# Kernel optimization log

Hardware: AMD Instinct MI355X
Metric: run time of the kernel (lower is better)

The kernel has to match this reference:

```python
import jax, jax.numpy as jnp
import numpy as np

N, P, C = 8, 256, 128


def setup_inputs() -> dict:
    key = jax.random.key(0)
    ks = jax.random.split(key, 16)
    s = lambda k, shape, fan_in: jax.random.normal(k, shape, jnp.float32) / np.sqrt(fan_in)
    return {
        "x": jax.random.normal(ks[0], (N, P, C), jnp.float32),
        "pos": jax.random.normal(ks[1], (N, P, P, 2), jnp.float32),
        # projections (no bias), stored (in, out)
        "Wq": s(ks[2], (C, C), C),
        "Wk": s(ks[3], (C, C), C),
        "Wv": s(ks[4], (C, C), C),
        # qk_mlp: Linear(C,C) -> ReLU -> Linear(C,1)
        "W1": s(ks[5], (C, C), C),
        "b1": jnp.zeros((C,), jnp.float32),
        "W2": s(ks[6], (C, 1), C),
        "b2": jnp.zeros((1,), jnp.float32),
        # pos_mlp: Linear(2,C) -> ReLU -> Linear(C,C)
        "Wp1": s(ks[7], (2, C), 2),
        "bp1": jnp.zeros((C,), jnp.float32),
        "Wp2": s(ks[8], (C, C), C),
        "bp2": jnp.zeros((C,), jnp.float32),
    }


def reference(x, pos, Wq, Wk, Wv, W1, b1, W2, b2, Wp1, bp1, Wp2, bp2):
    # x: [N,P,C], pos: [N,P,P,2]
    q = x @ Wq  # [N,P,C]
    k = x @ Wk
    v = x @ Wv
    pos_emb = jax.nn.relu(pos @ Wp1 + bp1) @ Wp2 + bp2  # [N,P,P,C]
    # diff[n,a,b,:] = q[n,b] - k[n,a] + pos_emb[n,a,b]
    diff = q[:, None, :, :] - k[:, :, None, :] + pos_emb  # [N,P,P,C]
    att = (jax.nn.relu(diff @ W1 + b1) @ W2 + b2)[..., 0]  # [N,P,P]
    att = jax.nn.softmax(att, axis=-1)
    # out[n,a] = sum_b att[n,a,b] * v[n,b]
    fuse = jnp.einsum("nab,nbc->nac", att, v)
    return x + fuse
```

## Files before the change

### kernel.cpp

```cpp
#include <hip/hip_runtime.h>
#include <hip/hip_bf16.h>

#define NB 8
#define PP 256
#define CC 128
#define APAD 136
#define XS 132

typedef __attribute__((ext_vector_type(8))) unsigned short ushort8;
typedef __bf16 bf16x8 __attribute__((ext_vector_type(8)));
typedef float float4v __attribute__((ext_vector_type(4)));

__device__ __forceinline__ float bf2f(unsigned short u) {
    union { unsigned int i; float f; } x; x.i = ((unsigned int)u) << 16; return x.f;
}
__device__ __forceinline__ unsigned short f2bf(float f) {
    union { float f; unsigned int i; } x; x.f = f;
    unsigned int r = x.i + 0x7fffu + ((x.i >> 16) & 1u);
    return (unsigned short)(r >> 16);
}
__device__ __forceinline__ unsigned int pk2(float a, float b) {
    return (unsigned int)f2bf(a) | ((unsigned int)f2bf(b) << 16);
}

__global__ void prep_kernel(const float* __restrict__ Wq, const float* __restrict__ Wk,
                            const float* __restrict__ Wp2, const float* __restrict__ W1,
                            const float* __restrict__ b1, const float* __restrict__ bp2,
                            float* __restrict__ Wq1, float* __restrict__ Wk1,
                            unsigned short* __restrict__ W21t, float* __restrict__ bvec) {
    int bx = blockIdx.x, j = threadIdx.x;
    __shared__ float xr[CC];
    if (bx < 384) {
        int r = bx & 127;
        const float* X = (bx < 128) ? Wq : (bx < 256) ? Wk : Wp2;
        xr[j] = X[r * CC + j];
        __syncthreads();
        float s = 0.f;
#pragma unroll 4
        for (int t = 0; t < CC; ++t) s = fmaf(xr[t], W1[t * CC + j], s);
        if (bx < 128)      Wq1[r * CC + j] = s;
        else if (bx < 256) Wk1[r * CC + j] = s;
        else               W21t[j * CC + r] = f2bf(s);
    } else {
        float s = b1[j];
        for (int c = 0; c < CC; ++c) s = fmaf(bp2[c], W1[c * CC + j], s);
        bvec[j] = s;
    }
}

__global__ __launch_bounds__(256) void qkv_kernel(
    const float* __restrict__ x, const float* __restrict__ Wq1,
    const float* __restrict__ Wk1, const float* __restrict__ Wv,
    unsigned short* __restrict__ qwtb, float* __restrict__ kw,
    float* __restrict__ v) {
    __shared__ float Ws[CC * CC];
    __shared__ float xs[32 * XS];
    int t = threadIdx.x, which = blockIdx.y;
    const float* W = (which == 0) ? Wq1 : (which == 1) ? Wk1 : Wv;
    int row0 = blockIdx.x * 32;
#pragma unroll 8
    for (int i = 0; i < 64; ++i) Ws[i * 256 + t] = W[i * 256 + t];
#pragma unroll 4
    for (int i = 0; i < 16; ++i) {
        int idx = i * 256 + t;
        int r = idx >> 7, c = idx & 127;
        xs[r * XS + c] = x[(size_t)(row0 + r) * CC + c];
    }
    __syncthreads();
    int tc = t & 31, tr = t >> 5;
    int j0 = tc * 4, r0 = tr * 4;
    float acc[4][4];
#pragma unroll
    for (int i = 0; i < 4; ++i)
#pragma unroll
        for (int jj = 0; jj < 4; ++jj) acc[i][jj] = 0.f;
#pragma unroll 2
    for (int c = 0; c < CC; ++c) {
        float4 w4 = *(const float4*)&Ws[c * CC + j0];
        float x0 = xs[(r0 + 0) * XS + c], x1 = xs[(r0 + 1) * XS + c];
        float x2 = xs[(r0 + 2) * XS + c], x3 = xs[(r0 + 3) * XS + c];
        acc[0][0] = fmaf(x0, w4.x, acc[0][0]); acc[0][1] = fmaf(x0, w4.y, acc[0][1]);
        acc[0][2] = fmaf(x0, w4.z, acc[0][2]); acc[0][3] = fmaf(x0, w4.w, acc[0][3]);
        acc[1][0] = fmaf(x1, w4.x, acc[1][0]); acc[1][1] = fmaf(x1, w4.y, acc[1][1]);
        acc[1][2] = fmaf(x1, w4.z, acc[1][2]); acc[1][3] = fmaf(x1, w4.w, acc[1][3]);
        acc[2][0] = fmaf(x2, w4.x, acc[2][0]); acc[2][1] = fmaf(x2, w4.y, acc[2][1]);
        acc[2][2] = fmaf(x2, w4.z, acc[2][2]); acc[2][3] = fmaf(x2, w4.w, acc[2][3]);
        acc[3][0] = fmaf(x3, w4.x, acc[3][0]); acc[3][1] = fmaf(x3, w4.y, acc[3][1]);
        acc[3][2] = fmaf(x3, w4.z, acc[3][2]); acc[3][3] = fmaf(x3, w4.w, acc[3][3]);
    }
    if (which == 0) {
        int n = row0 >> 8, b0 = row0 & 255;
#pragma unroll
        for (int jj = 0; jj < 4; ++jj) {
            ushort4 pk;
            pk.x = f2bf(acc[0][jj]); pk.y = f2bf(acc[1][jj]);
            pk.z = f2bf(acc[2][jj]); pk.w = f2bf(acc[3][jj]);
            *(ushort4*)(qwtb + (size_t)(n * CC + j0 + jj) * PP + b0 + r0) = pk;
        }
    } else {
        float* o = (which == 1) ? kw : v;
#pragma unroll
        for (int i = 0; i < 4; ++i)
            *(float4*)&o[(size_t)(row0 + r0 + i) * CC + j0] =
                make_float4(acc[i][0], acc[i][1], acc[i][2], acc[i][3]);
    }
}

__global__ __launch_bounds__(256, 3) void attn_kernel(
    const float* __restrict__ x, const float* __restrict__ pos,
    const float* __restrict__ Wp1, const float* __restrict__ bp1,
    const float* __restrict__ W2, const float* __restrict__ b2,
    const unsigned short* __restrict__ W21t, const float* __restrict__ bvec,
    const unsigned short* __restrict__ qwtb, const float* __restrict__ kw,
    const float* __restrict__ v, float* __restrict__ out)
{
    __shared__ __attribute__((aligned(16))) unsigned short Bs[128 * APAD];
    __shared__ float p0s[PP], p1s[PP];
    __shared__ float wa[CC], wb[CC], bpv[CC];
    __shared__ float logits[PP];
    __shared__ float red[8];
    __shared__ float avred[CC];

    const int t = threadIdx.x;
    const int n = blockIdx.x >> 8, a = blockIdx.x & 255;
    const int lane = t & 63, wv = t >> 6;
    const int ln = lane & 15, quad = lane >> 4;

    if (t < CC) {
        wa[t]  = Wp1[t];
        wb[t]  = Wp1[CC + t];
        bpv[t] = bp1[t];
    }
    {
        const float2* pr = (const float2*)(pos + (size_t)(n * PP + a) * PP * 2);
        float2 pp = pr[t];
        p0s[t] = pp.x;
        p1s[t] = pp.y;
    }
    {
        int j = t >> 1, p = t & 1;
        const ushort8* src = (const ushort8*)(W21t + j * CC + p * 64);
        ushort8* dst = (ushort8*)(Bs + j * APAD + p * 64);
#pragma unroll
        for (int i = 0; i < 8; ++i) dst[i] = src[i];
    }
    const float b2f = b2[0];

    float w2v[8], kbv[8];
    {
        const float* kwrow = kw + (size_t)(n * PP + a) * CC;
#pragma unroll
        for (int nt = 0; nt < 8; ++nt) {
            int j = nt * 16 + ln;
            w2v[nt] = W2[j];
            kbv[nt] = bvec[j] - kwrow[j];
        }
    }
    __syncthreads();

#pragma unroll 1
    for (int chunk = 0; chunk < 4; ++chunk) {
        const int rbase = chunk * 64 + wv * 16;
        const float P0 = p0s[rbase + ln];
        const float P1 = p1s[rbase + ln];

        ushort4 qv4[8];
#pragma unroll
        for (int nt = 0; nt < 8; ++nt)
            qv4[nt] = *(const ushort4*)(qwtb + (size_t)(n * CC + nt * 16 + ln) * PP
                                        + rbase + quad * 4);

        float4v acc[8];
#pragma unroll
        for (int j = 0; j < 8; ++j) acc[j] = (float4v)0.f;

#pragma unroll 1
        for (int kk = 0; kk < 128; kk += 32) {
            const int ko = kk + quad * 8;
            float4 a0 = *(const float4*)&wa[ko],  a1 = *(const float4*)&wa[ko + 4];
            float4 c0 = *(const float4*)&wb[ko],  c1 = *(const float4*)&wb[ko + 4];
            float4 d0 = *(const float4*)&bpv[ko], d1 = *(const float4*)&bpv[ko + 4];
            float h0 = fmaxf(fmaf(P0, a0.x, fmaf(P1, c0.x, d0.x)), 0.f);
            float h1 = fmaxf(fmaf(P0, a0.y, fmaf(P1, c0.y, d0.y)), 0.f);
            float h2 = fmaxf(fmaf(P0, a0.z, fmaf(P1, c0.z, d0.z)), 0.f);
            float h3 = fmaxf(fmaf(P0, a0.w, fmaf(P1, c0.w, d0.w)), 0.f);
            float h4 = fmaxf(fmaf(P0, a1.x, fmaf(P1, c1.x, d1.x)), 0.f);
            float h5 = fmaxf(fmaf(P0, a1.y, fmaf(P1, c1.y, d1.y)), 0.f);
            float h6 = fmaxf(fmaf(P0, a1.z, fmaf(P1, c1.z, d1.z)), 0.f);
            float h7 = fmaxf(fmaf(P0, a1.w, fmaf(P1, c1.w, d1.w)), 0.f);
            union { bf16x8 v8; unsigned int u[4]; } cv;
            cv.u[0] = pk2(h0, h1); cv.u[1] = pk2(h2, h3);
            cv.u[2] = pk2(h4, h5); cv.u[3] = pk2(h6, h7);
            bf16x8 af = cv.v8;
#pragma unroll
            for (int j = 0; j < 8; ++j) {
                bf16x8 bfr = *(const bf16x8*)(Bs + (j * 16 + ln) * APAD + ko);
                acc[j] = __builtin_amdgcn_mfma_f32_16x16x32_bf16(af, bfr, acc[j], 0, 0, 0);
            }
        }

        float s0 = 0.f, s1 = 0.f, s2 = 0.f, s3 = 0.f;
#pragma unroll
        for (int nt = 0; nt < 8; ++nt) {
            float kb = kbv[nt], w2 = w2v[nt];
            s0 = fmaf(fmaxf(acc[nt][0] + bf2f(qv4[nt].x) + kb, 0.f), w2, s0);
            s1 = fmaf(fmaxf(acc[nt][1] + bf2f(qv4[nt].y) + kb, 0.f), w2, s1);
            s2 = fmaf(fmaxf(acc[nt][2] + bf2f(qv4[nt].z) + kb, 0.f), w2, s2);
            s3 = fmaf(fmaxf(acc[nt][3] + bf2f(qv4[nt].w) + kb, 0.f), w2, s3);
        }
        float sr[4] = {s0, s1, s2, s3};
#pragma unroll
        for (int r = 0; r < 4; ++r) {
            float s = sr[r];
            s += __shfl_xor(s, 1);
            s += __shfl_xor(s, 2);
            s += __shfl_xor(s, 4);
            s += __shfl_xor(s, 8);
            if (ln == 0) logits[rbase + quad * 4 + r] = s + b2f;
        }
    }
    __syncthreads();

    float lv = logits[t];
    float wm = lv;
#pragma unroll
    for (int d = 1; d < 64; d <<= 1) wm = fmaxf(wm, __shfl_xor(wm, d));
    if (lane == 0) red[wv] = wm;
    __syncthreads();
    float m = fmaxf(fmaxf(red[0], red[1]), fmaxf(red[2], red[3]));
    float e = __expf(lv - m);
    float es = e;
#pragma unroll
    for (int d = 1; d < 64; d <<= 1) es += __shfl_xor(es, d);
    if (lane == 0) red[4 + wv] = es;
    __syncthreads();
    float denom = red[4] + red[5] + red[6] + red[7];
    logits[t] = e / denom;
    __syncthreads();

    int c = t & 127, h2 = t >> 7;
    const float* vp = v + (size_t)(n * PP + h2 * 128) * CC + c;
    float acc0 = 0.f;
#pragma unroll 8
    for (int b = 0; b < 128; ++b)
        acc0 = fmaf(logits[h2 * 128 + b], vp[(size_t)b * CC], acc0);
    if (h2 == 1) avred[c] = acc0;
    __syncthreads();
    if (h2 == 0) {
        int oidx = (n * PP + a) * CC + c;
        out[oidx] = x[oidx] + acc0 + avred[c];
    }
}

extern "C" void kernel_launch(void* const* d_in, const int* in_sizes, int n_in,
                              void* d_out, int out_size, void* d_ws, size_t ws_size,
                              hipStream_t stream) {
    const float* x   = (const float*)d_in[0];
    const float* pos = (const float*)d_in[1];
    const float* Wq  = (const float*)d_in[2];
    const float* Wk  = (const float*)d_in[3];
    const float* Wv  = (const float*)d_in[4];
    const float* W1  = (const float*)d_in[5];
    const float* b1  = (const float*)d_in[6];
    const float* W2  = (const float*)d_in[7];
    const float* b2  = (const float*)d_in[8];
    const float* Wp1 = (const float*)d_in[9];
    const float* bp1 = (const float*)d_in[10];
    const float* Wp2 = (const float*)d_in[11];
    const float* bp2 = (const float*)d_in[12];
    float* out = (float*)d_out;

    float* ws   = (float*)d_ws;
    float* Wq1  = ws;
    float* Wk1  = Wq1 + 16384;
    float* bvec = Wk1 + 16384;
    float* kw   = bvec + 128;
    float* v    = kw + 262144;
    unsigned short* qwtb = (unsigned short*)(v + 262144);
    unsigned short* W21t = qwtb + 262144;

    prep_kernel<<<385, 128, 0, stream>>>(Wq, Wk, Wp2, W1, b1, bp2, Wq1, Wk1, W21t, bvec);
    qkv_kernel<<<dim3(64, 3), 256, 0, stream>>>(x, Wq1, Wk1, Wv, qwtb, kw, v);
    attn_kernel<<<NB * PP, 256, 0, stream>>>(x, pos, Wp1, bp1, W2, b2,
                                             W21t, bvec, qwtb, kw, v, out);
}
```

Before: 158.7 us.

## Switch pos-MLP hidden to packed fp16 with pre-swizzled f16 MFMA weights

The pos-MLP first layer is now computed with packed half2 math, with weights held in registers. The combined W2·W1 matrix is stored in fp16, pre-swizzled by the prep kernel into MFMA fragment order, so the attention kernel can copy it linearly into LDS and read conflict-free without padding. This drops the fp32 FMA and bf16 rounding work and the strided LDS loads. The final attention-times-V step now splits the b dimension over 8 groups with float4 loads and reduces them through shared memory. The main risk is lower precision for pos and hidden values in fp16, plus higher register pressure from the per-thread weight arrays.

```diff
diff --git a/kernel.cpp b/kernel.cpp
--- a/kernel.cpp
+++ b/kernel.cpp
@@ -4,11 +4,11 @@
 #define NB 8
 #define PP 256
 #define CC 128
-#define APAD 136
 #define XS 132
 
 typedef __attribute__((ext_vector_type(8))) unsigned short ushort8;
-typedef __bf16 bf16x8 __attribute__((ext_vector_type(8)));
+typedef _Float16 f16x8 __attribute__((ext_vector_type(8)));
+typedef _Float16 h2v __attribute__((ext_vector_type(2)));
 typedef float float4v __attribute__((ext_vector_type(4)));
 
 __device__ __forceinline__ float bf2f(unsigned short u) {
@@ -19,15 +19,12 @@
     unsigned int r = x.i + 0x7fffu + ((x.i >> 16) & 1u);
     return (unsigned short)(r >> 16);
 }
-__device__ __forceinline__ unsigned int pk2(float a, float b) {
-    return (unsigned int)f2bf(a) | ((unsigned int)f2bf(b) << 16);
-}
 
 __global__ void prep_kernel(const float* __restrict__ Wq, const float* __restrict__ Wk,
                             const float* __restrict__ Wp2, const float* __restrict__ W1,
                             const float* __restrict__ b1, const float* __restrict__ bp2,
                             float* __restrict__ Wq1, float* __restrict__ Wk1,
-                            unsigned short* __restrict__ W21t, float* __restrict__ bvec) {
+                            unsigned short* __restrict__ W21f, float* __restrict__ bvec) {
     int bx = blockIdx.x, j = threadIdx.x;
     __shared__ float xr[CC];
     if (bx < 384) {
@@ -40,7 +37,15 @@
         for (int t = 0; t < CC; ++t) s = fmaf(xr[t], W1[t * CC + j], s);
         if (bx < 128)      Wq1[r * CC + j] = s;
         else if (bx < 256) Wk1[r * CC + j] = s;
-        else               W21t[j * CC + r] = f2bf(s);
+        else {
+            int k = r;
+            int kk = k >> 5, quad = (k >> 3) & 3, e = k & 7;
+            int jt = j >> 4, ln = j & 15;
+            int lane = quad * 16 + ln;
+            union { _Float16 h; unsigned short u; } cv;
+            cv.h = (_Float16)s;
+            W21f[(((kk * 8 + jt) * 64) + lane) * 8 + e] = cv.u;
+        }
     } else {
         float s = b1[j];
         for (int c = 0; c < CC; ++c) s = fmaf(bp2[c], W1[c * CC + j], s);
@@ -110,27 +115,21 @@
     const float* __restrict__ x, const float* __restrict__ pos,
     const float* __restrict__ Wp1, const float* __restrict__ bp1,
     const float* __restrict__ W2, const float* __restrict__ b2,
-    const unsigned short* __restrict__ W21t, const float* __restrict__ bvec,
+    const unsigned short* __restrict__ W21f, const float* __restrict__ bvec,
     const unsigned short* __restrict__ qwtb, const float* __restrict__ kw,
     const float* __restrict__ v, float* __restrict__ out)
 {
-    __shared__ __attribute__((aligned(16))) unsigned short Bs[128 * APAD];
+    __shared__ __attribute__((aligned(16))) unsigned short Bs[128 * 128];
     __shared__ float p0s[PP], p1s[PP];
-    __shared__ float wa[CC], wb[CC], bpv[CC];
     __shared__ float logits[PP];
     __shared__ float red[8];
-    __shared__ float avred[CC];
+    __shared__ float avp[8 * 128];
 
     const int t = threadIdx.x;
     const int n = blockIdx.x >> 8, a = blockIdx.x & 255;
     const int lane = t & 63, wv = t >> 6;
     const int ln = lane & 15, quad = lane >> 4;
 
-    if (t < CC) {
-        wa[t]  = Wp1[t];
-        wb[t]  = Wp1[CC + t];
-        bpv[t] = bp1[t];
-    }
     {
         const float2* pr = (const float2*)(pos + (size_t)(n * PP + a) * PP * 2);
         float2 pp = pr[t];
@@ -138,13 +137,23 @@
         p1s[t] = pp.y;
     }
     {
-        int j = t >> 1, p = t & 1;
-        const ushort8* src = (const ushort8*)(W21t + j * CC + p * 64);
-        ushort8* dst = (ushort8*)(Bs + j * APAD + p * 64);
-#pragma unroll
-        for (int i = 0; i < 8; ++i) dst[i] = src[i];
+        const uint4* src = (const uint4*)W21f;
+        uint4* dst = (uint4*)Bs;
+#pragma unroll
+        for (int i = 0; i < 8; ++i) dst[i * 256 + t] = src[i * 256 + t];
     }
     const float b2f = b2[0];
+
+    h2v wa2[16], wb2[16], bp2h[16];
+#pragma unroll
+    for (int kk = 0; kk < 4; ++kk)
+#pragma unroll
+        for (int p = 0; p < 4; ++p) {
+            int k = kk * 32 + quad * 8 + p * 2;
+            wa2[kk * 4 + p]  = (h2v){(_Float16)Wp1[k],      (_Float16)Wp1[k + 1]};
+            wb2[kk * 4 + p]  = (h2v){(_Float16)Wp1[CC + k], (_Float16)Wp1[CC + k + 1]};
+            bp2h[kk * 4 + p] = (h2v){(_Float16)bp1[k],      (_Float16)bp1[k + 1]};
+        }
 
     float w2v[8], kbv[8];
     {
@@ -156,13 +165,16 @@
             kbv[nt] = bvec[j] - kwrow[j];
         }
     }
+    const h2v z2 = (h2v){(_Float16)0.f, (_Float16)0.f};
     __syncthreads();
 
 #pragma unroll 1
     for (int chunk = 0; chunk < 4; ++chunk) {
         const int rbase = chunk * 64 + wv * 16;
-        const float P0 = p0s[rbase + ln];
-        const float P1 = p1s[rbase + ln];
+        const _Float16 p0h = (_Float16)p0s[rbase + ln];
+        const _Float16 p1h = (_Float16)p1s[rbase + ln];
+        const h2v P0h = (h2v){p0h, p0h};
+        const h2v P1h = (h2v){p1h, p1h};
 
         ushort4 qv4[8];
 #pragma unroll
@@ -175,27 +187,16 @@
         for (int j = 0; j < 8; ++j) acc[j] = (float4v)0.f;
 
 #pragma unroll 1
-        for (int kk = 0; kk < 128; kk += 32) {
-            const int ko = kk + quad * 8;
-            float4 a0 = *(const float4*)&wa[ko],  a1 = *(const float4*)&wa[ko + 4];
-            float4 c0 = *(const float4*)&wb[ko],  c1 = *(const float4*)&wb[ko + 4];
-            float4 d0 = *(const float4*)&bpv[ko], d1 = *(const float4*)&bpv[ko + 4];
-            float h0 = fmaxf(fmaf(P0, a0.x, fmaf(P1, c0.x, d0.x)), 0.f);
-            float h1 = fmaxf(fmaf(P0, a0.y, fmaf(P1, c0.y, d0.y)), 0.f);
-            float h2 = fmaxf(fmaf(P0, a0.z, fmaf(P1, c0.z, d0.z)), 0.f);
-            float h3 = fmaxf(fmaf(P0, a0.w, fmaf(P1, c0.w, d0.w)), 0.f);
-            float h4 = fmaxf(fmaf(P0, a1.x, fmaf(P1, c1.x, d1.x)), 0.f);
-            float h5 = fmaxf(fmaf(P0, a1.y, fmaf(P1, c1.y, d1.y)), 0.f);
-            float h6 = fmaxf(fmaf(P0, a1.z, fmaf(P1, c1.z, d1.z)), 0.f);
-            float h7 = fmaxf(fmaf(P0, a1.w, fmaf(P1, c1.w, d1.w)), 0.f);
-            union { bf16x8 v8; unsigned int u[4]; } cv;
-            cv.u[0] = pk2(h0, h1); cv.u[1] = pk2(h2, h3);
-            cv.u[2] = pk2(h4, h5); cv.u[3] = pk2(h6, h7);
-            bf16x8 af = cv.v8;
+        for (int kk = 0; kk < 4; ++kk) {
+            union { f16x8 v8; h2v h2[4]; } A;
+#pragma unroll
+            for (int p = 0; p < 4; ++p)
+                A.h2[p] = __builtin_elementwise_max(
+                    P0h * wa2[kk * 4 + p] + P1h * wb2[kk * 4 + p] + bp2h[kk * 4 + p], z2);
 #pragma unroll
             for (int j = 0; j < 8; ++j) {
-                bf16x8 bfr = *(const bf16x8*)(Bs + (j * 16 + ln) * APAD + ko);
-                acc[j] = __builtin_amdgcn_mfma_f32_16x16x32_bf16(af, bfr, acc[j], 0, 0, 0);
+                f16x8 bfr = *(const f16x8*)(Bs + (((kk * 8 + j) * 64) + lane) * 8);
+                acc[j] = __builtin_amdgcn_mfma_f32_16x16x32_f16(A.v8, bfr, acc[j], 0, 0, 0);
             }
         }
 
@@ -238,17 +239,26 @@
     logits[t] = e / denom;
     __syncthreads();
 
-    int c = t & 127, h2 = t >> 7;
-    const float* vp = v + (size_t)(n * PP + h2 * 128) * CC + c;
-    float acc0 = 0.f;
-#pragma unroll 8
-    for (int b = 0; b < 128; ++b)
-        acc0 = fmaf(logits[h2 * 128 + b], vp[(size_t)b * CC], acc0);
-    if (h2 == 1) avred[c] = acc0;
-    __syncthreads();
-    if (h2 == 0) {
-        int oidx = (n * PP + a) * CC + c;
-        out[oidx] = x[oidx] + acc0 + avred[c];
+    {
+        int c4 = (t & 31) * 4, bg = t >> 5;
+        const float* vp = v + (size_t)(n * PP + bg * 32) * CC + c4;
+        float4 av = make_float4(0.f, 0.f, 0.f, 0.f);
+#pragma unroll 4
+        for (int b = 0; b < 32; ++b) {
+            float w = logits[bg * 32 + b];
+            float4 vv = *(const float4*)(vp + (size_t)b * CC);
+            av.x = fmaf(w, vv.x, av.x); av.y = fmaf(w, vv.y, av.y);
+            av.z = fmaf(w, vv.z, av.z); av.w = fmaf(w, vv.w, av.w);
+        }
+        *(float4*)&avp[bg * 128 + c4] = av;
+    }
+    __syncthreads();
+    if (t < 128) {
+        int oidx = (n * PP + a) * CC + t;
+        float s = x[oidx];
+#pragma unroll
+        for (int g = 0; g < 8; ++g) s += avp[g * 128 + t];
+        out[oidx] = s;
     }
 }
 
@@ -277,10 +287,10 @@
     float* kw   = bvec + 128;
     float* v    = kw + 262144;
     unsigned short* qwtb = (unsigned short*)(v + 262144);
-    unsigned short* W21t = qwtb + 262144;
-
-    prep_kernel<<<385, 128, 0, stream>>>(Wq, Wk, Wp2, W1, b1, bp2, Wq1, Wk1, W21t, bvec);
+    unsigned short* W21f = qwtb + 262144;
+
+    prep_kernel<<<385, 128, 0, stream>>>(Wq, Wk, Wp2, W1, b1, bp2, Wq1, Wk1, W21f, bvec);
     qkv_kernel<<<dim3(64, 3), 256, 0, stream>>>(x, Wq1, Wk1, Wv, qwtb, kw, v);
     attn_kernel<<<NB * PP, 256, 0, stream>>>(x, pos, Wp1, bp1, W2, b2,
-                                             W21t, bvec, qwtb, kw, v, out);
-}
+                                             W21f, bvec, qwtb, kw, v, out);
+}
```

Measured after the change: 318.2 us. +100.5%, slower.
